# Performance work log

Hardware: AMD Instinct MI355X
Metric: run time of the kernel (lower is better)

Reference implementation:

```python
import jax, jax.numpy as jnp
import numpy as np
from jax import lax

DN = ('NCHW', 'OIHW', 'NCHW')


def setup_inputs() -> dict:
    key = jax.random.key(0)
    k1, k2 = jax.random.split(key)
    x = jax.random.uniform(k1, (32, 3, 128, 128), dtype=jnp.float32)
    # kaiming-uniform-like filters; the module zeroes the first filter after init
    fan_in = 1 * 7 * 7
    bound = np.sqrt(6.0 / ((1 + 5.0) * fan_in))  # kaiming_uniform with a=sqrt(5)
    weight = jax.random.uniform(k2, (512, 1, 7, 7), minval=-bound, maxval=bound,
                                dtype=jnp.float32)
    weight = weight.at[0].set(0.0)
    std = jnp.asarray(2.0, dtype=jnp.float32)
    return {"x": x, "weight": weight, "std": std}


def _rbf_dist_conv(gray, weight, std, stride=1):
    # ||window - filter||^2 = ||window||^2 + ||filter||^2 - 2 * window . filter
    strides = (stride, stride)
    xw = lax.conv_general_dilated(gray, weight, strides, 'VALID',
                                  dimension_numbers=DN)       # [B,O,OH,OW]
    ones_k = jnp.ones((1, 1) + weight.shape[2:], gray.dtype)
    x2 = lax.conv_general_dilated(gray * gray, ones_k, strides, 'VALID',
                                  dimension_numbers=DN)       # [B,1,OH,OW]
    w2 = jnp.sum(weight * weight, axis=(1, 2, 3))[None, :, None, None]
    sq = jnp.maximum(x2 + w2 - 2.0 * xw, 0.0)
    dist = jnp.sqrt(sq)                                        # torch.cdist
    # gauss RBF: exp(-d^2 / (2*std^2))
    return jnp.exp(-(dist * dist) / (2.0 * std * std))


def reference(x, weight, std):
    # forward converts 3-channel input to grayscale (ITU-R 601 weights, as torchvision)
    gray = (0.2989 * x[:, 0] + 0.587 * x[:, 1] + 0.114 * x[:, 2])[:, None]  # [B,1,H,W]
    return _rbf_dist_conv(gray, weight, std, stride=1)
```

## Files before the change

kernel.cpp:

```cpp
#include <hip/hip_runtime.h>

typedef _Float16 half_t;
typedef __attribute__((ext_vector_type(4))) _Float16 half4;
typedef __attribute__((ext_vector_type(8))) _Float16 half8;
typedef __attribute__((ext_vector_type(2))) float f32x2;
typedef __attribute__((ext_vector_type(4))) float f32x4;

#define NB 32
#define NH 128
#define NW 128
#define NOH 122
#define NOW 122
#define NOC 512
#define KPAD 64


__global__ __launch_bounds__(256) void k_gray(const float* __restrict__ x,
                                              half_t* __restrict__ gh) {
    int t = blockIdx.x * 256 + threadIdx.x;
    if (t >= NB * NH * NW / 4) return;
    int b = t >> 12;
    int pix4 = t & 4095;
    const float* xb = x + (size_t)b * 3 * 16384 + pix4 * 4;
    f32x4 r = *(const f32x4*)xb;
    f32x4 g = *(const f32x4*)(xb + 16384);
    f32x4 bl = *(const f32x4*)(xb + 32768);
    half4 o;
#pragma unroll
    for (int i = 0; i < 4; ++i)
        o[i] = (half_t)(0.2989f * r[i] + 0.587f * g[i] + 0.114f * bl[i]);
    *(half4*)(gh + (size_t)t * 4) = o;
}

__global__ __launch_bounds__(256) void k_w(const float* __restrict__ w,
                                           half_t* __restrict__ Wh,
                                           float* __restrict__ w2) {
    int o = blockIdx.x * 256 + threadIdx.x;
    if (o >= NOC) return;
    float s = 0.f;
    for (int t = 0; t < KPAD; ++t) {
        int kh = t >> 3, kw = t & 7;
        float v = (kh < 7 && kw < 7) ? w[o * 49 + kh * 7 + kw] : 0.f;
        half_t h = (half_t)v;
        Wh[o * KPAD + t] = h;
        float f = (float)h;
        s += f * f;
    }
    w2[o] = s;
}

__global__ __launch_bounds__(256) void k_rs(const half_t* __restrict__ gh,
                                            float* __restrict__ Sg) {
    int t = blockIdx.x * 256 + threadIdx.x;
    if (t >= NB * NH * NOW) return;
    int b = t / (NH * NOW);
    int rem = t - b * (NH * NOW);
    int h = rem / NOW;
    int p = rem - h * NOW;
    const half_t* g = gh + ((size_t)b * NH + h) * NW + p;
    float s = 0.f;
#pragma unroll
    for (int kw = 0; kw < 7; ++kw) {
        float v = (float)g[kw];
        s += v * v;
    }
    Sg[t] = s;
}

__global__ __launch_bounds__(256) void k_x2(const float* __restrict__ Sg,
                                            float* __restrict__ x2) {
    int t = blockIdx.x * 256 + threadIdx.x;
    if (t >= NB * NOH * NOW) return;
    int b = t / (NOH * NOW);
    int rem = t - b * (NOH * NOW);
    int oh = rem / NOW;
    int p = rem - oh * NOW;
    const float* s0 = Sg + ((size_t)b * NH + oh) * NOW + p;
    float s = 0.f;
#pragma unroll
    for (int kh = 0; kh < 7; ++kh) s += s0[kh * NOW];
    x2[t] = s;
}

__global__ __launch_bounds__(256) void k_main(const half_t* __restrict__ gh,
                                              const half_t* __restrict__ Wh,
                                              const float* __restrict__ w2,
                                              const float* __restrict__ x2,
                                              const float* __restrict__ stdp,
                                              float* __restrict__ out) {
    const int ohp = blockIdx.x;
    const int fgg = blockIdx.y;
    const int b   = blockIdx.z;
    const int oh0 = ohp * 2;

    __shared__ half_t gS[9][136];
    __shared__ float  outT[32 * 244];

    const int tid  = threadIdx.x;
    const int wave = tid >> 6;
    const int lane = tid & 63;
    const int col  = lane & 15;
    const int kq   = lane >> 4;
    const int n0   = wave * 32;

    for (int idx = tid; idx < 9 * 136; idx += 256) {
        int r = idx / 136;
        int c = idx - r * 136;
        int row = oh0 + r;
        if (row > NH - 1) row = NH - 1;
        gS[r][c] = (c < 128) ? gh[((size_t)b * NH + row) * NW + c] : (half_t)0.f;
    }

    half8 wfrag[2][2];
#pragma unroll
    for (int ni = 0; ni < 2; ++ni)
#pragma unroll
        for (int ks = 0; ks < 2; ++ks)
            wfrag[ni][ks] = *(const half8*)(Wh + ((size_t)(fgg * 32 + ni * 16 + col) * KPAD
                                                  + (ks * 4 + kq) * 8));
    float w2c[2];
#pragma unroll
    for (int ni = 0; ni < 2; ++ni) w2c[ni] = w2[fgg * 32 + ni * 16 + col];

    const float sv = stdp[0];
    const float inv2s2 = 0.5f / (sv * sv);

    __syncthreads();

#pragma unroll
    for (int lo = 0; lo < 2; ++lo) {
        const int oh = oh0 + lo;

        half8 afrag[2][2];
#pragma unroll
        for (int mi = 0; mi < 2; ++mi) {
            const int p = n0 + mi * 16 + col;
#pragma unroll
            for (int ks = 0; ks < 2; ++ks) {
                const half_t* src = &gS[lo + ks * 4 + kq][p];
                half8 v;
#pragma unroll
                for (int i = 0; i < 8; ++i) v[i] = src[i];
                afrag[mi][ks] = v;
            }
        }

        f32x4 acc[2][2];
#pragma unroll
        for (int mi = 0; mi < 2; ++mi)
#pragma unroll
            for (int ni = 0; ni < 2; ++ni) {
                f32x4 z = {0.f, 0.f, 0.f, 0.f};
                acc[mi][ni] = z;
            }

#pragma unroll
        for (int ks = 0; ks < 2; ++ks)
#pragma unroll
            for (int mi = 0; mi < 2; ++mi)
#pragma unroll
                for (int ni = 0; ni < 2; ++ni)
                    acc[mi][ni] = __builtin_amdgcn_mfma_f32_16x16x32_f16(
                        afrag[mi][ks], wfrag[ni][ks], acc[mi][ni], 0, 0, 0);

        const size_t rowBase = ((size_t)b * NOH + oh) * NOW;

#pragma unroll
        for (int mi = 0; mi < 2; ++mi) {
            const int p0 = n0 + mi * 16 + kq * 4;
            if (p0 >= NOW) continue;
            const f32x4 x2v = *(const f32x4*)(x2 + rowBase + p0);
            const bool full = (p0 + 3 < NOW);
#pragma unroll
            for (int ni = 0; ni < 2; ++ni) {
                f32x4 res;
#pragma unroll
                for (int r = 0; r < 4; ++r) {
                    float sq = fmaxf(fmaf(-2.f, acc[mi][ni][r], x2v[r] + w2c[ni]), 0.f);
                    res[r] = __expf(-sq * inv2s2);
                }
                float* dst = &outT[(ni * 16 + col) * 244 + lo * 122 + p0];
                f32x2 lo2 = {res[0], res[1]};
                *(f32x2*)dst = lo2;
                if (full) {
                    f32x2 hi2 = {res[2], res[3]};
                    *(f32x2*)(dst + 2) = hi2;
                }
            }
        }
    }

    __syncthreads();

    if (lane < 61) {
        const size_t base = (((size_t)b * NOC + fgg * 32) * NOH + oh0) * NOW;
#pragma unroll 4
        for (int c = 0; c < 8; ++c) {
            const int o = wave * 8 + c;
            f32x4 v = *(const f32x4*)&outT[o * 244 + lane * 4];
            __builtin_nontemporal_store(v, (f32x4*)(out + base + (size_t)o * NOH * NOW + lane * 4));
        }
    }
}

extern "C" void kernel_launch(void* const* d_in, const int* in_sizes, int n_in,
                              void* d_out, int out_size, void* d_ws, size_t ws_size,
                              hipStream_t stream) {
    const float* x    = (const float*)d_in[0];
    const float* w    = (const float*)d_in[1];
    const float* stdp = (const float*)d_in[2];
    float* out = (float*)d_out;

    char* ws = (char*)d_ws;
    half_t* gh = (half_t*)ws;
    half_t* Wh = (half_t*)(ws + 1048576);
    float*  w2 = (float*)(ws + 1114112);
    float*  x2 = (float*)(ws + 1116160);
    float*  Sg = (float*)(ws + 3021440);

    k_gray<<<(NB * NH * NW / 4 + 255) / 256, 256, 0, stream>>>(x, gh);
    k_w<<<(NOC + 255) / 256, 256, 0, stream>>>(w, Wh, w2);
    k_rs<<<(NB * NH * NOW + 255) / 256, 256, 0, stream>>>(gh, Sg);
    k_x2<<<(NB * NOH * NOW + 255) / 256, 256, 0, stream>>>(Sg, x2);

    dim3 grid(61, 16, NB);
    k_main<<<grid, 256, 0, stream>>>(gh, Wh, w2, x2, stdp, out);
}
```

Measured before the change: 332.2 us.

## Precompute shifted gray copies and process eight output rows per block

A new pre-pass kernel writes eight column-shifted copies of the fp16 grayscale image. The main kernel can then load each MFMA A-fragment as one aligned half8 global read, replacing the LDS staging tile and the per-element gathers. Each block now covers eight output rows in four steps instead of two rows, with a double-buffered output tile so the transpose-and-store needs only one barrier per step. The cost is an extra kernel and about 8x the grayscale footprint in workspace. The last row group overlaps its neighbour and rewrites some rows, and some reads land past the image or buffer ends but are multiplied by zero padded weights.

```diff
diff --git a/kernel.cpp b/kernel.cpp
--- a/kernel.cpp
+++ b/kernel.cpp
@@ -13,12 +13,13 @@
 #define NOW 122
 #define NOC 512
 #define KPAD 64
+#define NPIX (NB * NH * NW)
 
 
 __global__ __launch_bounds__(256) void k_gray(const float* __restrict__ x,
                                               half_t* __restrict__ gh) {
     int t = blockIdx.x * 256 + threadIdx.x;
-    if (t >= NB * NH * NW / 4) return;
+    if (t >= NPIX / 4) return;
     int b = t >> 12;
     int pix4 = t & 4095;
     const float* xb = x + (size_t)b * 3 * 16384 + pix4 * 4;
@@ -49,6 +50,23 @@
     w2[o] = s;
 }
 
+__global__ __launch_bounds__(256) void k_shift(const half_t* __restrict__ gh,
+                                               half_t* __restrict__ ghs) {
+    int t = blockIdx.x * 256 + threadIdx.x;
+    if (t >= NPIX / 8) return;
+    const half8* g8 = (const half8*)gh;
+    half8 a0 = g8[t];
+    half8 a1 = g8[t + 1];
+#pragma unroll
+    for (int s = 0; s < 8; ++s) {
+        half8 v;
+#pragma unroll
+        for (int i = 0; i < 8; ++i)
+            v[i] = (i + s < 8) ? a0[i + s] : a1[i + s - 8];
+        *(half8*)(ghs + (size_t)s * NPIX + (size_t)t * 8) = v;
+    }
+}
+
 __global__ __launch_bounds__(256) void k_rs(const half_t* __restrict__ gh,
                                             float* __restrict__ Sg) {
     int t = blockIdx.x * 256 + threadIdx.x;
@@ -82,19 +100,18 @@
     x2[t] = s;
 }
 
-__global__ __launch_bounds__(256) void k_main(const half_t* __restrict__ gh,
+__global__ __launch_bounds__(256) void k_main(const half_t* __restrict__ ghs,
                                               const half_t* __restrict__ Wh,
                                               const float* __restrict__ w2,
                                               const float* __restrict__ x2,
                                               const float* __restrict__ stdp,
                                               float* __restrict__ out) {
-    const int ohp = blockIdx.x;
+    const int ohg = blockIdx.x;
     const int fgg = blockIdx.y;
     const int b   = blockIdx.z;
-    const int oh0 = ohp * 2;
-
-    __shared__ half_t gS[9][136];
-    __shared__ float  outT[32 * 244];
+    const int oh0 = (ohg * 8 > NOH - 8) ? (NOH - 8) : (ohg * 8);
+
+    __shared__ float outT[2][32 * 244];
 
     const int tid  = threadIdx.x;
     const int wave = tid >> 6;
@@ -103,13 +120,9 @@
     const int kq   = lane >> 4;
     const int n0   = wave * 32;
 
-    for (int idx = tid; idx < 9 * 136; idx += 256) {
-        int r = idx / 136;
-        int c = idx - r * 136;
-        int row = oh0 + r;
-        if (row > NH - 1) row = NH - 1;
-        gS[r][c] = (c < 128) ? gh[((size_t)b * NH + row) * NW + c] : (half_t)0.f;
-    }
+    const int s = col & 7;
+    const half_t* gsh = ghs + (size_t)s * NPIX;
+    const int pb0 = n0 + (col & 8);
 
     half8 wfrag[2][2];
 #pragma unroll
@@ -125,80 +138,80 @@
     const float sv = stdp[0];
     const float inv2s2 = 0.5f / (sv * sv);
 
-    __syncthreads();
-
-#pragma unroll
-    for (int lo = 0; lo < 2; ++lo) {
-        const int oh = oh0 + lo;
-
-        half8 afrag[2][2];
-#pragma unroll
-        for (int mi = 0; mi < 2; ++mi) {
-            const int p = n0 + mi * 16 + col;
-#pragma unroll
-            for (int ks = 0; ks < 2; ++ks) {
-                const half_t* src = &gS[lo + ks * 4 + kq][p];
-                half8 v;
-#pragma unroll
-                for (int i = 0; i < 8; ++i) v[i] = src[i];
-                afrag[mi][ks] = v;
+    for (int q = 0; q < 4; ++q) {
+        float* buf = outT[q & 1];
+
+#pragma unroll
+        for (int lo2 = 0; lo2 < 2; ++lo2) {
+            const int oh = oh0 + q * 2 + lo2;
+
+            half8 afrag[2][2];
+#pragma unroll
+            for (int mi = 0; mi < 2; ++mi) {
+#pragma unroll
+                for (int ks = 0; ks < 2; ++ks) {
+                    const int row = oh + ks * 4 + kq;
+                    const size_t flat = ((size_t)(b * NH + row)) * NW + pb0 + mi * 16;
+                    afrag[mi][ks] = *(const half8*)(gsh + flat);
+                }
             }
-        }
-
-        f32x4 acc[2][2];
-#pragma unroll
-        for (int mi = 0; mi < 2; ++mi)
-#pragma unroll
-            for (int ni = 0; ni < 2; ++ni) {
-                f32x4 z = {0.f, 0.f, 0.f, 0.f};
-                acc[mi][ni] = z;
-            }
-
-#pragma unroll
-        for (int ks = 0; ks < 2; ++ks)
+
+            f32x4 acc[2][2];
 #pragma unroll
             for (int mi = 0; mi < 2; ++mi)
 #pragma unroll
-                for (int ni = 0; ni < 2; ++ni)
-                    acc[mi][ni] = __builtin_amdgcn_mfma_f32_16x16x32_f16(
-                        afrag[mi][ks], wfrag[ni][ks], acc[mi][ni], 0, 0, 0);
-
-        const size_t rowBase = ((size_t)b * NOH + oh) * NOW;
-
-#pragma unroll
-        for (int mi = 0; mi < 2; ++mi) {
-            const int p0 = n0 + mi * 16 + kq * 4;
-            if (p0 >= NOW) continue;
-            const f32x4 x2v = *(const f32x4*)(x2 + rowBase + p0);
-            const bool full = (p0 + 3 < NOW);
-#pragma unroll
-            for (int ni = 0; ni < 2; ++ni) {
-                f32x4 res;
-#pragma unroll
-                for (int r = 0; r < 4; ++r) {
-                    float sq = fmaxf(fmaf(-2.f, acc[mi][ni][r], x2v[r] + w2c[ni]), 0.f);
-                    res[r] = __expf(-sq * inv2s2);
+                for (int ni = 0; ni < 2; ++ni) {
+                    f32x4 z = {0.f, 0.f, 0.f, 0.f};
+                    acc[mi][ni] = z;
                 }
-                float* dst = &outT[(ni * 16 + col) * 244 + lo * 122 + p0];
-                f32x2 lo2 = {res[0], res[1]};
-                *(f32x2*)dst = lo2;
-                if (full) {
-                    f32x2 hi2 = {res[2], res[3]};
-                    *(f32x2*)(dst + 2) = hi2;
+
+#pragma unroll
+            for (int ks = 0; ks < 2; ++ks)
+#pragma unroll
+                for (int mi = 0; mi < 2; ++mi)
+#pragma unroll
+                    for (int ni = 0; ni < 2; ++ni)
+                        acc[mi][ni] = __builtin_amdgcn_mfma_f32_16x16x32_f16(
+                            afrag[mi][ks], wfrag[ni][ks], acc[mi][ni], 0, 0, 0);
+
+            const size_t rowBase = ((size_t)b * NOH + oh) * NOW;
+
+#pragma unroll
+            for (int mi = 0; mi < 2; ++mi) {
+                const int p0 = n0 + mi * 16 + kq * 4;
+                if (p0 >= NOW) continue;
+                const f32x4 x2v = *(const f32x4*)(x2 + rowBase + p0);
+                const bool full = (p0 + 3 < NOW);
+#pragma unroll
+                for (int ni = 0; ni < 2; ++ni) {
+                    f32x4 res;
+#pragma unroll
+                    for (int r = 0; r < 4; ++r) {
+                        float sq = fmaxf(fmaf(-2.f, acc[mi][ni][r], x2v[r] + w2c[ni]), 0.f);
+                        res[r] = __expf(-sq * inv2s2);
+                    }
+                    float* dst = &buf[(ni * 16 + col) * 244 + lo2 * 122 + p0];
+                    f32x2 lo2v = {res[0], res[1]};
+                    *(f32x2*)dst = lo2v;
+                    if (full) {
+                        f32x2 hi2 = {res[2], res[3]};
+                        *(f32x2*)(dst + 2) = hi2;
+                    }
                 }
             }
         }
-    }
-
-    __syncthreads();
-
-    if (lane < 61) {
-        const size_t base = (((size_t)b * NOC + fgg * 32) * NOH + oh0) * NOW;
+
+        __syncthreads();
+
+        if (lane < 61) {
+            const size_t base = (((size_t)b * NOC + fgg * 32) * NOH + (oh0 + q * 2)) * NOW;
 #pragma unroll 4
-        for (int c = 0; c < 8; ++c) {
-            const int o = wave * 8 + c;
-            f32x4 v = *(const f32x4*)&outT[o * 244 + lane * 4];
-            __builtin_nontemporal_store(v, (f32x4*)(out + base + (size_t)o * NOH * NOW + lane * 4));
+            for (int c = 0; c < 8; ++c) {
+                const int o = wave * 8 + c;
+                f32x4 v = *(const f32x4*)&buf[o * 244 + lane * 4];
+                __builtin_nontemporal_store(
+                    v, (f32x4*)(out + base + (size_t)o * NOH * NOW + lane * 4));
+            }
         }
     }
 }
@@ -212,17 +225,19 @@
     float* out = (float*)d_out;
 
     char* ws = (char*)d_ws;
-    half_t* gh = (half_t*)ws;
-    half_t* Wh = (half_t*)(ws + 1048576);
-    float*  w2 = (float*)(ws + 1114112);
-    float*  x2 = (float*)(ws + 1116160);
-    float*  Sg = (float*)(ws + 3021440);
-
-    k_gray<<<(NB * NH * NW / 4 + 255) / 256, 256, 0, stream>>>(x, gh);
+    half_t* gh  = (half_t*)ws;
+    half_t* Wh  = (half_t*)(ws + 1048576);
+    float*  w2  = (float*)(ws + 1114112);
+    float*  x2  = (float*)(ws + 1116160);
+    float*  Sg  = (float*)(ws + 3021440);
+    half_t* ghs = (half_t*)(ws + 5020288);
+
+    k_gray<<<(NPIX / 4 + 255) / 256, 256, 0, stream>>>(x, gh);
     k_w<<<(NOC + 255) / 256, 256, 0, stream>>>(w, Wh, w2);
+    k_shift<<<(NPIX / 8 + 255) / 256, 256, 0, stream>>>(gh, ghs);
     k_rs<<<(NB * NH * NOW + 255) / 256, 256, 0, stream>>>(gh, Sg);
     k_x2<<<(NB * NOH * NOW + 255) / 256, 256, 0, stream>>>(Sg, x2);
 
-    dim3 grid(61, 16, NB);
-    k_main<<<grid, 256, 0, stream>>>(gh, Wh, w2, x2, stdp, out);
-}
+    dim3 grid(16, 16, NB);
+    k_main<<<grid, 256, 0, stream>>>(ghs, Wh, w2, x2, stdp, out);
+}
```

Result: slower. 339.4 us (+2.2%).

## Process eight output rows per block with double-buffered LDS output staging

Applied to the files above, without the earlier changes.

Each k_main block now covers eight output rows instead of two, in four iterations of two rows each. It loads 15 grayscale rows and the weight fragments once per block, so that per-block setup is amortised. The output tile alternates between two LDS buffers, and the full-block barrier is replaced by an lgkmcnt wait plus s_barrier, so the MFMA/exp work for the next row pair can overlap the global stores of the previous one. The last row group is clamped, so it recomputes and rewrites some rows another block also writes. The doubled LDS footprint lowers the number of resident blocks per CU.

```diff
diff --git a/kernel.cpp b/kernel.cpp
--- a/kernel.cpp
+++ b/kernel.cpp
@@ -88,13 +88,13 @@
                                               const float* __restrict__ x2,
                                               const float* __restrict__ stdp,
                                               float* __restrict__ out) {
-    const int ohp = blockIdx.x;
+    const int ohg = blockIdx.x;
     const int fgg = blockIdx.y;
     const int b   = blockIdx.z;
-    const int oh0 = ohp * 2;
-
-    __shared__ half_t gS[9][136];
-    __shared__ float  outT[32 * 244];
+    const int oh0 = (ohg * 8 > NOH - 8) ? (NOH - 8) : (ohg * 8);
+
+    __shared__ half_t gS[15][136];
+    __shared__ float  outT[2][32 * 244];
 
     const int tid  = threadIdx.x;
     const int wave = tid >> 6;
@@ -103,7 +103,7 @@
     const int kq   = lane >> 4;
     const int n0   = wave * 32;
 
-    for (int idx = tid; idx < 9 * 136; idx += 256) {
+    for (int idx = tid; idx < 15 * 136; idx += 256) {
         int r = idx / 136;
         int c = idx - r * 136;
         int row = oh0 + r;
@@ -127,78 +127,86 @@
 
     __syncthreads();
 
-#pragma unroll
-    for (int lo = 0; lo < 2; ++lo) {
-        const int oh = oh0 + lo;
-
-        half8 afrag[2][2];
-#pragma unroll
-        for (int mi = 0; mi < 2; ++mi) {
-            const int p = n0 + mi * 16 + col;
-#pragma unroll
-            for (int ks = 0; ks < 2; ++ks) {
-                const half_t* src = &gS[lo + ks * 4 + kq][p];
-                half8 v;
-#pragma unroll
-                for (int i = 0; i < 8; ++i) v[i] = src[i];
-                afrag[mi][ks] = v;
+    for (int q = 0; q < 4; ++q) {
+        float* buf = outT[q & 1];
+
+#pragma unroll
+        for (int lo2 = 0; lo2 < 2; ++lo2) {
+            const int ohr = q * 2 + lo2;
+            const int oh  = oh0 + ohr;
+
+            half8 afrag[2][2];
+#pragma unroll
+            for (int mi = 0; mi < 2; ++mi) {
+                const int p = n0 + mi * 16 + col;
+#pragma unroll
+                for (int ks = 0; ks < 2; ++ks) {
+                    const half_t* src = &gS[ohr + ks * 4 + kq][p];
+                    half8 v;
+#pragma unroll
+                    for (int i = 0; i < 8; ++i) v[i] = src[i];
+                    afrag[mi][ks] = v;
+                }
             }
-        }
-
-        f32x4 acc[2][2];
-#pragma unroll
-        for (int mi = 0; mi < 2; ++mi)
-#pragma unroll
-            for (int ni = 0; ni < 2; ++ni) {
-                f32x4 z = {0.f, 0.f, 0.f, 0.f};
-                acc[mi][ni] = z;
-            }
-
-#pragma unroll
-        for (int ks = 0; ks < 2; ++ks)
+
+            f32x4 acc[2][2];
 #pragma unroll
             for (int mi = 0; mi < 2; ++mi)
 #pragma unroll
-                for (int ni = 0; ni < 2; ++ni)
-                    acc[mi][ni] = __builtin_amdgcn_mfma_f32_16x16x32_f16(
-                        afrag[mi][ks], wfrag[ni][ks], acc[mi][ni], 0, 0, 0);
-
-        const size_t rowBase = ((size_t)b * NOH + oh) * NOW;
-
-#pragma unroll
-        for (int mi = 0; mi < 2; ++mi) {
-            const int p0 = n0 + mi * 16 + kq * 4;
-            if (p0 >= NOW) continue;
-            const f32x4 x2v = *(const f32x4*)(x2 + rowBase + p0);
-            const bool full = (p0 + 3 < NOW);
-#pragma unroll
-            for (int ni = 0; ni < 2; ++ni) {
-                f32x4 res;
-#pragma unroll
-                for (int r = 0; r < 4; ++r) {
-                    float sq = fmaxf(fmaf(-2.f, acc[mi][ni][r], x2v[r] + w2c[ni]), 0.f);
-                    res[r] = __expf(-sq * inv2s2);
+                for (int ni = 0; ni < 2; ++ni) {
+                    f32x4 z = {0.f, 0.f, 0.f, 0.f};
+                    acc[mi][ni] = z;
                 }
-                float* dst = &outT[(ni * 16 + col) * 244 + lo * 122 + p0];
-                f32x2 lo2 = {res[0], res[1]};
-                *(f32x2*)dst = lo2;
-                if (full) {
-                    f32x2 hi2 = {res[2], res[3]};
-                    *(f32x2*)(dst + 2) = hi2;
+
+#pragma unroll
+            for (int ks = 0; ks < 2; ++ks)
+#pragma unroll
+                for (int mi = 0; mi < 2; ++mi)
+#pragma unroll
+                    for (int ni = 0; ni < 2; ++ni)
+                        acc[mi][ni] = __builtin_amdgcn_mfma_f32_16x16x32_f16(
+                            afrag[mi][ks], wfrag[ni][ks], acc[mi][ni], 0, 0, 0);
+
+            const size_t rowBase = ((size_t)b * NOH + oh) * NOW;
+
+#pragma unroll
+            for (int mi = 0; mi < 2; ++mi) {
+                const int p0 = n0 + mi * 16 + kq * 4;
+                if (p0 >= NOW) continue;
+                const f32x4 x2v = *(const f32x4*)(x2 + rowBase + p0);
+                const bool full = (p0 + 3 < NOW);
+#pragma unroll
+                for (int ni = 0; ni < 2; ++ni) {
+                    f32x4 res;
+#pragma unroll
+                    for (int r = 0; r < 4; ++r) {
+                        float sq = fmaxf(fmaf(-2.f, acc[mi][ni][r], x2v[r] + w2c[ni]), 0.f);
+                        res[r] = __expf(-sq * inv2s2);
+                    }
+                    float* dst = &buf[(ni * 16 + col) * 244 + lo2 * 122 + p0];
+                    f32x2 lo2v = {res[0], res[1]};
+                    *(f32x2*)dst = lo2v;
+                    if (full) {
+                        f32x2 hi2 = {res[2], res[3]};
+                        *(f32x2*)(dst + 2) = hi2;
+                    }
                 }
             }
         }
-    }
-
-    __syncthreads();
-
-    if (lane < 61) {
-        const size_t base = (((size_t)b * NOC + fgg * 32) * NOH + oh0) * NOW;
+
+        asm volatile("s_waitcnt lgkmcnt(0)" ::: "memory");
+        __builtin_amdgcn_sched_barrier(0);
+        __builtin_amdgcn_s_barrier();
+
+        if (lane < 61) {
+            const size_t base = (((size_t)b * NOC + fgg * 32) * NOH + (oh0 + q * 2)) * NOW;
 #pragma unroll 4
-        for (int c = 0; c < 8; ++c) {
-            const int o = wave * 8 + c;
-            f32x4 v = *(const f32x4*)&outT[o * 244 + lane * 4];
-            __builtin_nontemporal_store(v, (f32x4*)(out + base + (size_t)o * NOH * NOW + lane * 4));
+            for (int c = 0; c < 8; ++c) {
+                const int o = wave * 8 + c;
+                f32x4 v = *(const f32x4*)&buf[o * 244 + lane * 4];
+                __builtin_nontemporal_store(
+                    v, (f32x4*)(out + base + (size_t)o * NOH * NOW + lane * 4));
+            }
         }
     }
 }
@@ -223,6 +231,6 @@
     k_rs<<<(NB * NH * NOW + 255) / 256, 256, 0, stream>>>(gh, Sg);
     k_x2<<<(NB * NOH * NOW + 255) / 256, 256, 0, stream>>>(Sg, x2);
 
-    dim3 grid(61, 16, NB);
+    dim3 grid(16, 16, NB);
     k_main<<<grid, 256, 0, stream>>>(gh, Wh, w2, x2, stdp, out);
 }
```

Result: no change. 335.7 us (+1.0%).
